# Kernel tuning notes

Hardware: AMD Instinct MI355X
Metric: run time of the kernel (lower is better)

## Reference

```python
import jax, jax.numpy as jnp
import numpy as np

R, C, B, E, H = 128, 256, 1, 768, 12
DK = E // H

def setup_inputs() -> dict:
    key = jax.random.key(0)
    ks = jax.random.split(key, 5)
    s = 1.0 / np.sqrt(E)
    return {
        "x": jax.random.normal(ks[0], (R, C, B, E), jnp.float32),
        "Wq": jax.random.normal(ks[1], (E, E), jnp.float32) * s,
        "bq": jnp.zeros((E,), jnp.float32),
        "Wk": jax.random.normal(ks[2], (E, E), jnp.float32) * s,
        "bk": jnp.zeros((E,), jnp.float32),
        "Wv": jax.random.normal(ks[3], (E, E), jnp.float32) * s,
        "bv": jnp.zeros((E,), jnp.float32),
        "Wo": jax.random.normal(ks[4], (E, E), jnp.float32) * s,
        "bo": jnp.zeros((E,), jnp.float32),
    }

def reference(x, Wq, bq, Wk, bk, Wv, bv, Wo, bo):
    n_rows, n_cols, batch, emb = x.shape
    scaling = (DK ** -0.5) / jnp.sqrt(jnp.float32(n_rows))
    # projections (torch Linear: x @ W.T + b)
    q = (x @ Wq.T + bq).reshape(n_rows, n_cols, batch, H, DK) * scaling
    k = (x @ Wk.T + bk).reshape(n_rows, n_cols, batch, H, DK)
    v = (x @ Wv.T + bv).reshape(n_rows, n_cols, batch, H, DK)
    # pooled attention logits: sum over rows r -> [H, B, C, C]
    attn = jnp.einsum('rinhd,rjnhd->hnij', q, k)
    probs = jax.nn.softmax(attn, axis=-1)  # single softmax shared across rows
    # context: [R, C, B, H, DK]
    c = jnp.einsum('hnij,rjnhd->rinhd', probs, v).reshape(n_rows, n_cols, batch, emb)
    out = c @ Wo.T + bo
    return out, probs
```

## Files before the change

kernel.cpp:

```cpp
#include <hip/hip_runtime.h>
#include <math.h>

#define R_  128
#define C_  256
#define E_  768
#define H_  12
#define DK_ 64
#define T_  (R_*C_)
#define RS_ 8
#define LP  40

typedef __attribute__((ext_vector_type(8))) short          bf16x8;
typedef __attribute__((ext_vector_type(4))) float          f32x4;
typedef __attribute__((ext_vector_type(4))) unsigned short u16x4;
typedef __attribute__((ext_vector_type(8))) unsigned short u16x8;

struct HL { unsigned short h, l; };

__device__ __forceinline__ HL split2(float f) {
    HL o;
    unsigned int u = __float_as_uint(f);
    o.h = (unsigned short)(u >> 16);
    float r = f - __uint_as_float(u & 0xFFFF0000u);
    o.l = (unsigned short)(__float_as_uint(r) >> 16);
    return o;
}

__device__ __forceinline__ void gload16(const void* g, void* l) {
    __builtin_amdgcn_global_load_lds(
        (const __attribute__((address_space(1))) unsigned int*)g,
        (__attribute__((address_space(3))) unsigned int*)l,
        16, 0, 0);
}

__global__ __launch_bounds__(256) void split_kernel(
    const float* __restrict__ src,
    unsigned short* __restrict__ h, unsigned short* __restrict__ l)
{
    const size_t i = ((size_t)blockIdx.x * 256 + threadIdx.x) * 8;
    float4 f0 = *(const float4*)(src + i);
    float4 f1 = *(const float4*)(src + i + 4);
    float v[8] = { f0.x, f0.y, f0.z, f0.w, f1.x, f1.y, f1.z, f1.w };
    u16x8 hh, ll;
    #pragma unroll
    for (int j = 0; j < 8; ++j) { HL e = split2(v[j]); hh[j] = e.h; ll[j] = e.l; }
    *(u16x8*)(h + i) = hh;
    *(u16x8*)(l + i) = ll;
}

template<int OMODE>
__global__ __launch_bounds__(256, 2) void gemm_kernel(
    const unsigned short* __restrict__ Ah, const unsigned short* __restrict__ Al,
    const unsigned short* __restrict__ Bh, const unsigned short* __restrict__ Bl,
    const float* __restrict__ bias, float scale,
    float* __restrict__ Y32, unsigned short* __restrict__ Yh, unsigned short* __restrict__ Yl)
{
    __shared__ __align__(16) unsigned short smem[2][16384];

    const int tid  = threadIdx.x;
    const int m0   = blockIdx.x * 128;
    const int n0   = blockIdx.y * 128;
    const int wave = tid >> 6, lane = tid & 63;
    const int wm   = (wave & 1) * 64, wn = (wave >> 1) * 64;
    const int fr   = lane & 15;
    const int kqs  = (((lane >> 4) ^ ((fr >> 1) & 3)) * 8);

    const int lrow = lane >> 2;
    const int gd   = (lane & 3) ^ ((lane >> 3) & 3);
    const unsigned short* gsrc = (wave == 0) ? Ah : (wave == 1) ? Al
                               : (wave == 2) ? Bh : Bl;
    const int rbase = (wave < 2) ? m0 : n0;
    const unsigned short* sp = gsrc + (size_t)(rbase + lrow) * E_ + 8 * gd;
    const int ltoff = wave * 4096;

    f32x4 acc[4][4] = {};

    {
        unsigned short* lt = &smem[0][ltoff];
        #pragma unroll
        for (int i = 0; i < 8; ++i)
            gload16(sp + (size_t)i * 16 * E_, lt + i * 512);
    }

    int cur = 0;
    for (int k0 = 0; k0 < E_; k0 += 32) {
        __syncthreads();
        if (k0 + 32 < E_) {
            unsigned short* lt = &smem[cur ^ 1][ltoff];
            #pragma unroll
            for (int i = 0; i < 8; ++i)
                gload16(sp + k0 + 32 + (size_t)i * 16 * E_, lt + i * 512);
        }
        const unsigned short* AsH = smem[cur];
        const unsigned short* AsL = smem[cur] + 4096;
        const unsigned short* BsH = smem[cur] + 8192;
        const unsigned short* BsL = smem[cur] + 12288;

        bf16x8 a_h[4], a_l[4], b_h[4], b_l[4];
        #pragma unroll
        for (int t = 0; t < 4; ++t) {
            a_h[t] = *(const bf16x8*)&AsH[(wm + t * 16 + fr) * 32 + kqs];
            a_l[t] = *(const bf16x8*)&AsL[(wm + t * 16 + fr) * 32 + kqs];
            b_h[t] = *(const bf16x8*)&BsH[(wn + t * 16 + fr) * 32 + kqs];
            b_l[t] = *(const bf16x8*)&BsL[(wn + t * 16 + fr) * 32 + kqs];
        }
        #pragma unroll
        for (int i = 0; i < 4; ++i)
            #pragma unroll
            for (int j = 0; j < 4; ++j) {
                acc[i][j] = __builtin_amdgcn_mfma_f32_16x16x32_bf16(a_h[i], b_h[j], acc[i][j], 0, 0, 0);
                acc[i][j] = __builtin_amdgcn_mfma_f32_16x16x32_bf16(a_h[i], b_l[j], acc[i][j], 0, 0, 0);
                acc[i][j] = __builtin_amdgcn_mfma_f32_16x16x32_bf16(a_l[i], b_h[j], acc[i][j], 0, 0, 0);
            }
        cur ^= 1;
    }

    float* rep = (float*)&smem[0][0] + wave * 1024;
    const int mr = lane >> 2;
    const int nc = (lane & 3) * 16;
    #pragma unroll
    for (int ti = 0; ti < 4; ++ti) {
        __syncthreads();
        #pragma unroll
        for (int tj = 0; tj < 4; ++tj)
            #pragma unroll
            for (int r = 0; r < 4; ++r)
                rep[((lane >> 4) * 4 + r) * 64 + tj * 16 + fr] = acc[ti][tj][r];
        __syncthreads();
        float v[16];
        #pragma unroll
        for (int c = 0; c < 4; ++c)
            *(float4*)&v[4 * c] = *(const float4*)&rep[mr * 64 + nc + 4 * c];
        const int gm = m0 + wm + ti * 16 + mr;
        const int gn = n0 + wn + nc;
        if constexpr (OMODE == 1) {
            #pragma unroll
            for (int c = 0; c < 4; ++c) {
                float4 bv = *(const float4*)&bias[gn + 4 * c];
                float4 o;
                o.x = (v[4*c+0] + bv.x) * scale; o.y = (v[4*c+1] + bv.y) * scale;
                o.z = (v[4*c+2] + bv.z) * scale; o.w = (v[4*c+3] + bv.w) * scale;
                *(float4*)&Y32[(size_t)gm * E_ + gn + 4 * c] = o;
            }
        } else {
            unsigned short hh[16], ll[16];
            #pragma unroll
            for (int c = 0; c < 4; ++c) {
                float4 bv = *(const float4*)&bias[gn + 4 * c];
                HL e0 = split2((v[4*c+0] + bv.x) * scale);
                HL e1 = split2((v[4*c+1] + bv.y) * scale);
                HL e2 = split2((v[4*c+2] + bv.z) * scale);
                HL e3 = split2((v[4*c+3] + bv.w) * scale);
                hh[4*c+0] = e0.h; ll[4*c+0] = e0.l;
                hh[4*c+1] = e1.h; ll[4*c+1] = e1.l;
                hh[4*c+2] = e2.h; ll[4*c+2] = e2.l;
                hh[4*c+3] = e3.h; ll[4*c+3] = e3.l;
            }
            u16x8 H0, H1, L0, L1;
            #pragma unroll
            for (int j = 0; j < 8; ++j) { H0[j] = hh[j]; H1[j] = hh[8+j]; L0[j] = ll[j]; L1[j] = ll[8+j]; }
            *(u16x8*)&Yh[(size_t)gm * E_ + gn]     = H0;
            *(u16x8*)&Yh[(size_t)gm * E_ + gn + 8] = H1;
            *(u16x8*)&Yl[(size_t)gm * E_ + gn]     = L0;
            *(u16x8*)&Yl[(size_t)gm * E_ + gn + 8] = L1;
        }
    }
}

__global__ __launch_bounds__(256, 2) void attn_mfma(
    const unsigned short* __restrict__ Qh, const unsigned short* __restrict__ Ql,
    const unsigned short* __restrict__ Kh, const unsigned short* __restrict__ Kl,
    float* __restrict__ part)
{
    __shared__ __align__(16) unsigned short smem[2][16384];

    const int tid  = threadIdx.x;
    const int i0   = blockIdx.x * 128;
    const int j0   = blockIdx.y * 128;
    const int hz   = blockIdx.z;
    const int h    = hz >> 3;
    const int rc   = hz & 7;
    const int wave = tid >> 6, lane = tid & 63;
    const int wm   = (wave & 1) * 64, wn = (wave >> 1) * 64;
    const int fr   = lane & 15;
    const int kqs  = (((lane >> 4) ^ ((fr >> 1) & 3)) * 8);

    const int lrow = lane >> 2;
    const int gd   = (lane & 3) ^ ((lane >> 3) & 3);
    const unsigned short* gsrc = (wave == 0) ? Qh : (wave == 1) ? Ql
                               : (wave == 2) ? Kh : Kl;
    const int rbase = (wave < 2) ? i0 : j0;
    const int ltoff = wave * 4096;
    const unsigned short* sp0 =
        gsrc + ((size_t)(rc * 16 * C_) + rbase + lrow) * E_ + h * DK_ + 8 * gd;

    f32x4 acc[4][4] = {};

    {
        unsigned short* lt = &smem[0][ltoff];
        #pragma unroll
        for (int i = 0; i < 8; ++i)
            gload16(sp0 + (size_t)i * 16 * E_, lt + i * 512);
    }

    int cur = 0;
    for (int s = 0; s < 32; ++s) {
        __syncthreads();
        if (s + 1 < 32) {
            const int sn = s + 1;
            const unsigned short* sp =
                sp0 + (size_t)(sn >> 1) * C_ * E_ + (sn & 1) * 32;
            unsigned short* lt = &smem[cur ^ 1][ltoff];
            #pragma unroll
            for (int i = 0; i < 8; ++i)
                gload16(sp + (size_t)i * 16 * E_, lt + i * 512);
        }
        const unsigned short* AsH = smem[cur];
        const unsigned short* AsL = smem[cur] + 4096;
        const unsigned short* BsH = smem[cur] + 8192;
        const unsigned short* BsL = smem[cur] + 12288;

        bf16x8 a_h[4], a_l[4], b_h[4], b_l[4];
        #pragma unroll
        for (int t = 0; t < 4; ++t) {
            a_h[t] = *(const bf16x8*)&AsH[(wm + t * 16 + fr) * 32 + kqs];
            a_l[t] = *(const bf16x8*)&AsL[(wm + t * 16 + fr) * 32 + kqs];
            b_h[t] = *(const bf16x8*)&BsH[(wn + t * 16 + fr) * 32 + kqs];
            b_l[t] = *(const bf16x8*)&BsL[(wn + t * 16 + fr) * 32 + kqs];
        }
        #pragma unroll
        for (int i = 0; i < 4; ++i)
            #pragma unroll
            for (int j = 0; j < 4; ++j) {
                acc[i][j] = __builtin_amdgcn_mfma_f32_16x16x32_bf16(a_h[i], b_h[j], acc[i][j], 0, 0, 0);
                acc[i][j] = __builtin_amdgcn_mfma_f32_16x16x32_bf16(a_h[i], b_l[j], acc[i][j], 0, 0, 0);
                acc[i][j] = __builtin_amdgcn_mfma_f32_16x16x32_bf16(a_l[i], b_h[j], acc[i][j], 0, 0, 0);
            }
        cur ^= 1;
    }

    float* rep = (float*)&smem[0][0] + wave * 1024;
    const int mr = lane >> 2;
    const int nc = (lane & 3) * 16;
    #pragma unroll
    for (int ti = 0; ti < 4; ++ti) {
        __syncthreads();
        #pragma unroll
        for (int tj = 0; tj < 4; ++tj)
            #pragma unroll
            for (int r = 0; r < 4; ++r)
                rep[((lane >> 4) * 4 + r) * 64 + tj * 16 + fr] = acc[ti][tj][r];
        __syncthreads();
        const int gi = i0 + wm + ti * 16 + mr;
        const int gj = j0 + wn + nc;
        #pragma unroll
        for (int c = 0; c < 4; ++c) {
            float4 o = *(const float4*)&rep[mr * 64 + nc + 4 * c];
            *(float4*)&part[((size_t)(rc * H_ + h) * C_ + gi) * C_ + gj + 4 * c] = o;
        }
    }
}

__global__ __launch_bounds__(256) void softmax_split(
    const float* __restrict__ part, float* __restrict__ probs,
    unsigned short* __restrict__ ph, unsigned short* __restrict__ pl)
{
    const int row = blockIdx.x;
    const int j = threadIdx.x;
    const int wave = j >> 6, lane = j & 63;

    float s = 0.0f;
    #pragma unroll
    for (int rcn = 0; rcn < RS_; ++rcn)
        s += part[((size_t)rcn * H_ * C_ + row) * C_ + j];

    float m = s;
    #pragma unroll
    for (int off = 32; off > 0; off >>= 1)
        m = fmaxf(m, __shfl_down(m, off, 64));
    __shared__ float redm[4];
    if (lane == 0) redm[wave] = m;
    __syncthreads();
    m = fmaxf(fmaxf(redm[0], redm[1]), fmaxf(redm[2], redm[3]));

    float e = expf(s - m);
    float t = e;
    #pragma unroll
    for (int off = 32; off > 0; off >>= 1)
        t += __shfl_down(t, off, 64);
    __shared__ float reds[4];
    if (lane == 0) reds[wave] = t;
    __syncthreads();
    t = reds[0] + reds[1] + reds[2] + reds[3];

    float p = e / t;
    probs[(size_t)row * C_ + j] = p;
    HL sp = split2(p);
    ph[(size_t)row * C_ + j] = sp.h;
    pl[(size_t)row * C_ + j] = sp.l;
}

__global__ __launch_bounds__(256, 2) void ctx_mfma(
    const unsigned short* __restrict__ Ph, const unsigned short* __restrict__ Pl,
    const unsigned short* __restrict__ Vh, const unsigned short* __restrict__ Vl,
    unsigned short* __restrict__ Ch, unsigned short* __restrict__ Cl)
{
    __shared__ __align__(16) unsigned short smem[15360];
    unsigned short* PsH = smem;
    unsigned short* PsL = smem + 5120;
    unsigned short* VsH = smem + 10240;
    unsigned short* VsL = smem + 12800;

    const int tid  = threadIdx.x;
    const int i0   = blockIdx.x * 128;
    const int r    = blockIdx.y;
    const int h    = blockIdx.z;
    const int wave = tid >> 6, lane = tid & 63;
    const int wm   = (wave & 1) * 64, wn = (wave >> 1) * 32;
    const int fr   = lane & 15;
    const int kq   = (lane >> 4) * 8;
    const int srow = tid >> 1;
    const int sk   = (tid & 1) * 16;
    const int vjj  = tid & 31;
    const int vdg  = tid >> 5;

    f32x4 acc[4][2] = {};

    for (int s = 0; s < 8; ++s) {
        const int jb = s * 32;
        const size_t pb = ((size_t)(h * C_) + i0 + srow) * C_ + jb + sk;
        *(u16x8*)&PsH[srow * LP + sk]     = *(const u16x8*)&Ph[pb];
        *(u16x8*)&PsH[srow * LP + sk + 8] = *(const u16x8*)&Ph[pb + 8];
        *(u16x8*)&PsL[srow * LP + sk]     = *(const u16x8*)&Pl[pb];
        *(u16x8*)&PsL[srow * LP + sk + 8] = *(const u16x8*)&Pl[pb + 8];
        const size_t vb = ((size_t)(r * C_) + jb + vjj) * E_ + h * DK_ + vdg * 8;
        u16x8 v_h = *(const u16x8*)&Vh[vb];
        u16x8 v_l = *(const u16x8*)&Vl[vb];
        #pragma unroll
        for (int u = 0; u < 8; ++u) {
            VsH[(vdg * 8 + u) * LP + vjj] = v_h[u];
            VsL[(vdg * 8 + u) * LP + vjj] = v_l[u];
        }
        __syncthreads();

        bf16x8 p_h[4], p_l[4], w_h[2], w_l[2];
        #pragma unroll
        for (int t = 0; t < 4; ++t) {
            p_h[t] = *(const bf16x8*)&PsH[(wm + t * 16 + fr) * LP + kq];
            p_l[t] = *(const bf16x8*)&PsL[(wm + t * 16 + fr) * LP + kq];
        }
        #pragma unroll
        for (int t = 0; t < 2; ++t) {
            w_h[t] = *(const bf16x8*)&VsH[(wn + t * 16 + fr) * LP + kq];
            w_l[t] = *(const bf16x8*)&VsL[(wn + t * 16 + fr) * LP + kq];
        }
        #pragma unroll
        for (int i = 0; i < 4; ++i)
            #pragma unroll
            for (int j = 0; j < 2; ++j) {
                acc[i][j] = __builtin_amdgcn_mfma_f32_16x16x32_bf16(p_h[i], w_h[j], acc[i][j], 0, 0, 0);
                acc[i][j] = __builtin_amdgcn_mfma_f32_16x16x32_bf16(p_h[i], w_l[j], acc[i][j], 0, 0, 0);
                acc[i][j] = __builtin_amdgcn_mfma_f32_16x16x32_bf16(p_l[i], w_h[j], acc[i][j], 0, 0, 0);
            }
        __syncthreads();
    }

    float* rep = (float*)smem + wave * 512;
    const int mr = lane >> 2;
    const int nc = (lane & 3) * 8;
    #pragma unroll
    for (int ti = 0; ti < 4; ++ti) {
        __syncthreads();
        #pragma unroll
        for (int tj = 0; tj < 2; ++tj)
            #pragma unroll
            for (int rr = 0; rr < 4; ++rr)
                rep[((lane >> 4) * 4 + rr) * 32 + tj * 16 + fr] = acc[ti][tj][rr];
        __syncthreads();
        float v[8];
        *(float4*)&v[0] = *(const float4*)&rep[mr * 32 + nc];
        *(float4*)&v[4] = *(const float4*)&rep[mr * 32 + nc + 4];
        const int gm = r * C_ + i0 + wm + ti * 16 + mr;
        const int gn = h * DK_ + wn + nc;
        u16x8 H8, L8;
        #pragma unroll
        for (int jj = 0; jj < 8; ++jj) { HL e = split2(v[jj]); H8[jj] = e.h; L8[jj] = e.l; }
        *(u16x8*)&Ch[(size_t)gm * E_ + gn] = H8;
        *(u16x8*)&Cl[(size_t)gm * E_ + gn] = L8;
    }
}

extern "C" void kernel_launch(void* const* d_in, const int* in_sizes, int n_in,
                              void* d_out, int out_size, void* d_ws, size_t ws_size,
                              hipStream_t stream)
{
    (void)in_sizes; (void)n_in; (void)out_size; (void)ws_size;

    const float* x  = (const float*)d_in[0];
    const float* Wq = (const float*)d_in[1];
    const float* bq = (const float*)d_in[2];
    const float* Wk = (const float*)d_in[3];
    const float* bk = (const float*)d_in[4];
    const float* Wv = (const float*)d_in[5];
    const float* bv = (const float*)d_in[6];
    const float* Wo = (const float*)d_in[7];
    const float* bo = (const float*)d_in[8];

    float* out   = (float*)d_out;
    float* probs = out + (size_t)T_ * E_;
    float* part  = out;

    const size_t QN = (size_t)T_ * E_;
    const size_t WN = (size_t)E_ * E_;
    unsigned short* qh = (unsigned short*)d_ws;
    unsigned short* ql = qh + QN;
    unsigned short* kh = ql + QN;
    unsigned short* kl = kh + QN;
    unsigned short* vh = kl + QN;
    unsigned short* vl = vh + QN;
    unsigned short* ph = kh;
    unsigned short* pl = kh + (size_t)H_ * C_ * C_;
    unsigned short* ch = qh;
    unsigned short* cl = ql;

    unsigned short* xh   = (unsigned short*)out;
    unsigned short* xl   = xh + QN;
    unsigned short* wsph = (unsigned short*)probs;
    unsigned short* wspl = wsph + WN;
    unsigned short* woh  = kl;
    unsigned short* wol  = kl + WN;

    const float scaling = 0.125f / sqrtf(128.0f);

    dim3 blk(256);
    const int xblocks = (int)(QN / 2048);
    const int wblocks = (int)(WN / 2048);

    split_kernel<<<dim3(xblocks), blk, 0, stream>>>(x, xh, xl);

    split_kernel<<<dim3(wblocks), blk, 0, stream>>>(Wq, wsph, wspl);
    gemm_kernel<0><<<dim3(T_ / 128, E_ / 128), blk, 0, stream>>>(
        xh, xl, wsph, wspl, bq, scaling, nullptr, qh, ql);

    split_kernel<<<dim3(wblocks), blk, 0, stream>>>(Wk, wsph, wspl);
    gemm_kernel<0><<<dim3(T_ / 128, E_ / 128), blk, 0, stream>>>(
        xh, xl, wsph, wspl, bk, 1.0f, nullptr, kh, kl);

    split_kernel<<<dim3(wblocks), blk, 0, stream>>>(Wv, wsph, wspl);
    gemm_kernel<0><<<dim3(T_ / 128, E_ / 128), blk, 0, stream>>>(
        xh, xl, wsph, wspl, bv, 1.0f, nullptr, vh, vl);

    attn_mfma<<<dim3(C_ / 128, C_ / 128, H_ * RS_), blk, 0, stream>>>(qh, ql, kh, kl, part);

    split_kernel<<<dim3(wblocks), blk, 0, stream>>>(Wo, woh, wol);

    softmax_split<<<dim3(H_ * C_), blk, 0, stream>>>(part, probs, ph, pl);
    ctx_mfma<<<dim3(C_ / 128, R_, H_), blk, 0, stream>>>(ph, pl, vh, vl, ch, cl);

    gemm_kernel<1><<<dim3(T_ / 128, E_ / 128), blk, 0, stream>>>(
        ch, cl, woh, wol, bo, 1.0f, out, nullptr, nullptr);
}
```

Measured before the change: 873.6 us.

## Prefetch two stages ahead with explicit vmcnt waits in GEMM and logits kernels

Restructures the double-buffered main loops of the projection GEMM and the pooled-logits kernel so that two K-tiles are in flight at once. Each iteration waits on partial vmcnt instead of a full __syncthreads drain, reads fragments into registers, then barriers and refills the same buffer with tile t+2 before the MFMAs run. This aims to hide more global-to-LDS latency behind compute, at the cost of an extra barrier per iteration and reliance on hand-placed waitcnt correctness.

```diff
diff --git a/kernel.cpp b/kernel.cpp
--- a/kernel.cpp
+++ b/kernel.cpp
@@ -33,6 +33,11 @@
         16, 0, 0);
 }
 
+#define WAIT_VM8()   asm volatile("s_waitcnt vmcnt(8)"   ::: "memory")
+#define WAIT_VM0()   asm volatile("s_waitcnt vmcnt(0)"   ::: "memory")
+#define WAIT_LGKM0() asm volatile("s_waitcnt lgkmcnt(0)" ::: "memory")
+#define SBAR()       __builtin_amdgcn_s_barrier()
+
 __global__ __launch_bounds__(256) void split_kernel(
     const float* __restrict__ src,
     unsigned short* __restrict__ h, unsigned short* __restrict__ l)
@@ -76,21 +81,22 @@
     f32x4 acc[4][4] = {};
 
     {
-        unsigned short* lt = &smem[0][ltoff];
+        unsigned short* lt0 = &smem[0][ltoff];
         #pragma unroll
         for (int i = 0; i < 8; ++i)
-            gload16(sp + (size_t)i * 16 * E_, lt + i * 512);
-    }
-
-    int cur = 0;
-    for (int k0 = 0; k0 < E_; k0 += 32) {
-        __syncthreads();
-        if (k0 + 32 < E_) {
-            unsigned short* lt = &smem[cur ^ 1][ltoff];
-            #pragma unroll
-            for (int i = 0; i < 8; ++i)
-                gload16(sp + k0 + 32 + (size_t)i * 16 * E_, lt + i * 512);
-        }
+            gload16(sp + (size_t)i * 16 * E_, lt0 + i * 512);
+        unsigned short* lt1 = &smem[1][ltoff];
+        #pragma unroll
+        for (int i = 0; i < 8; ++i)
+            gload16(sp + 32 + (size_t)i * 16 * E_, lt1 + i * 512);
+    }
+
+    const int NT = E_ / 32;
+    for (int t = 0; t < NT; ++t) {
+        if (t < NT - 1) { WAIT_VM8(); } else { WAIT_VM0(); }
+        SBAR();
+
+        const int cur = t & 1;
         const unsigned short* AsH = smem[cur];
         const unsigned short* AsL = smem[cur] + 4096;
         const unsigned short* BsH = smem[cur] + 8192;
@@ -98,12 +104,23 @@
 
         bf16x8 a_h[4], a_l[4], b_h[4], b_l[4];
         #pragma unroll
-        for (int t = 0; t < 4; ++t) {
-            a_h[t] = *(const bf16x8*)&AsH[(wm + t * 16 + fr) * 32 + kqs];
-            a_l[t] = *(const bf16x8*)&AsL[(wm + t * 16 + fr) * 32 + kqs];
-            b_h[t] = *(const bf16x8*)&BsH[(wn + t * 16 + fr) * 32 + kqs];
-            b_l[t] = *(const bf16x8*)&BsL[(wn + t * 16 + fr) * 32 + kqs];
-        }
+        for (int u = 0; u < 4; ++u) {
+            a_h[u] = *(const bf16x8*)&AsH[(wm + u * 16 + fr) * 32 + kqs];
+            a_l[u] = *(const bf16x8*)&AsL[(wm + u * 16 + fr) * 32 + kqs];
+            b_h[u] = *(const bf16x8*)&BsH[(wn + u * 16 + fr) * 32 + kqs];
+            b_l[u] = *(const bf16x8*)&BsL[(wn + u * 16 + fr) * 32 + kqs];
+        }
+        WAIT_LGKM0();
+        SBAR();
+
+        if (t + 2 < NT) {
+            unsigned short* lt = &smem[cur][ltoff];
+            const unsigned short* spn = sp + (t + 2) * 32;
+            #pragma unroll
+            for (int i = 0; i < 8; ++i)
+                gload16(spn + (size_t)i * 16 * E_, lt + i * 512);
+        }
+
         #pragma unroll
         for (int i = 0; i < 4; ++i)
             #pragma unroll
@@ -112,7 +129,6 @@
                 acc[i][j] = __builtin_amdgcn_mfma_f32_16x16x32_bf16(a_h[i], b_l[j], acc[i][j], 0, 0, 0);
                 acc[i][j] = __builtin_amdgcn_mfma_f32_16x16x32_bf16(a_l[i], b_h[j], acc[i][j], 0, 0, 0);
             }
-        cur ^= 1;
     }
 
     float* rep = (float*)&smem[0][0] + wave * 1024;
@@ -197,24 +213,21 @@
     f32x4 acc[4][4] = {};
 
     {
-        unsigned short* lt = &smem[0][ltoff];
+        unsigned short* lt0 = &smem[0][ltoff];
         #pragma unroll
         for (int i = 0; i < 8; ++i)
-            gload16(sp0 + (size_t)i * 16 * E_, lt + i * 512);
-    }
-
-    int cur = 0;
-    for (int s = 0; s < 32; ++s) {
-        __syncthreads();
-        if (s + 1 < 32) {
-            const int sn = s + 1;
-            const unsigned short* sp =
-                sp0 + (size_t)(sn >> 1) * C_ * E_ + (sn & 1) * 32;
-            unsigned short* lt = &smem[cur ^ 1][ltoff];
-            #pragma unroll
-            for (int i = 0; i < 8; ++i)
-                gload16(sp + (size_t)i * 16 * E_, lt + i * 512);
-        }
+            gload16(sp0 + (size_t)i * 16 * E_, lt0 + i * 512);
+        unsigned short* lt1 = &smem[1][ltoff];
+        #pragma unroll
+        for (int i = 0; i < 8; ++i)
+            gload16(sp0 + 32 + (size_t)i * 16 * E_, lt1 + i * 512);
+    }
+
+    for (int t = 0; t < 32; ++t) {
+        if (t < 31) { WAIT_VM8(); } else { WAIT_VM0(); }
+        SBAR();
+
+        const int cur = t & 1;
         const unsigned short* AsH = smem[cur];
         const unsigned short* AsL = smem[cur] + 4096;
         const unsigned short* BsH = smem[cur] + 8192;
@@ -222,12 +235,25 @@
 
         bf16x8 a_h[4], a_l[4], b_h[4], b_l[4];
         #pragma unroll
-        for (int t = 0; t < 4; ++t) {
-            a_h[t] = *(const bf16x8*)&AsH[(wm + t * 16 + fr) * 32 + kqs];
-            a_l[t] = *(const bf16x8*)&AsL[(wm + t * 16 + fr) * 32 + kqs];
-            b_h[t] = *(const bf16x8*)&BsH[(wn + t * 16 + fr) * 32 + kqs];
-            b_l[t] = *(const bf16x8*)&BsL[(wn + t * 16 + fr) * 32 + kqs];
-        }
+        for (int u = 0; u < 4; ++u) {
+            a_h[u] = *(const bf16x8*)&AsH[(wm + u * 16 + fr) * 32 + kqs];
+            a_l[u] = *(const bf16x8*)&AsL[(wm + u * 16 + fr) * 32 + kqs];
+            b_h[u] = *(const bf16x8*)&BsH[(wn + u * 16 + fr) * 32 + kqs];
+            b_l[u] = *(const bf16x8*)&BsL[(wn + u * 16 + fr) * 32 + kqs];
+        }
+        WAIT_LGKM0();
+        SBAR();
+
+        if (t + 2 < 32) {
+            const int sn = t + 2;
+            const unsigned short* spn =
+                sp0 + (size_t)(sn >> 1) * C_ * E_ + (sn & 1) * 32;
+            unsigned short* lt = &smem[cur][ltoff];
+            #pragma unroll
+            for (int i = 0; i < 8; ++i)
+                gload16(spn + (size_t)i * 16 * E_, lt + i * 512);
+        }
+
         #pragma unroll
         for (int i = 0; i < 4; ++i)
             #pragma unroll
@@ -236,7 +262,6 @@
                 acc[i][j] = __builtin_amdgcn_mfma_f32_16x16x32_bf16(a_h[i], b_l[j], acc[i][j], 0, 0, 0);
                 acc[i][j] = __builtin_amdgcn_mfma_f32_16x16x32_bf16(a_l[i], b_h[j], acc[i][j], 0, 0, 0);
             }
-        cur ^= 1;
     }
 
     float* rep = (float*)&smem[0][0] + wave * 1024;
```

New measurement: 922.4 us. +5.6%, slower.

## Fuse weight hi/lo splitting into GEMM and merge QKV projections into one launch

Applied to the files above, without the earlier changes.

The GEMM now reads fp32 weights directly, splits them into bf16 hi/lo pairs on the fly, and writes them into shared memory. This removes the four separate weight-split kernels. The Q, K and V projections become a single launch with an 18-wide y grid that picks the weight, bias, scale and output per block. The cost is more per-thread conversion work and fp32 weight reads inside the K loop, done through register staging rather than async global-to-LDS loads, which may stall the pipeline.

```diff
diff --git a/kernel.cpp b/kernel.cpp
--- a/kernel.cpp
+++ b/kernel.cpp
@@ -49,48 +49,88 @@
 }
 
 template<int OMODE>
-__global__ __launch_bounds__(256, 2) void gemm_kernel(
+__global__ __launch_bounds__(256, 2) void gemm_fused(
     const unsigned short* __restrict__ Ah, const unsigned short* __restrict__ Al,
-    const unsigned short* __restrict__ Bh, const unsigned short* __restrict__ Bl,
-    const float* __restrict__ bias, float scale,
-    float* __restrict__ Y32, unsigned short* __restrict__ Yh, unsigned short* __restrict__ Yl)
+    const float* __restrict__ W0, const float* __restrict__ W1, const float* __restrict__ W2,
+    const float* __restrict__ b0, const float* __restrict__ b1, const float* __restrict__ b2,
+    float qscale, float* __restrict__ Y32,
+    unsigned short* __restrict__ Y0h, unsigned short* __restrict__ Y0l,
+    unsigned short* __restrict__ Y1h, unsigned short* __restrict__ Y1l,
+    unsigned short* __restrict__ Y2h, unsigned short* __restrict__ Y2l)
 {
     __shared__ __align__(16) unsigned short smem[2][16384];
 
-    const int tid  = threadIdx.x;
-    const int m0   = blockIdx.x * 128;
-    const int n0   = blockIdx.y * 128;
+    const int tid = threadIdx.x;
+    const int m0  = blockIdx.x * 128;
+    const int yb  = blockIdx.y;
+    const int sel = yb / 6;
+    const int n0  = (yb % 6) * 128;
+
+    const float* Wsel = (sel == 0) ? W0 : (sel == 1) ? W1 : W2;
+    const float* bsel = (sel == 0) ? b0 : (sel == 1) ? b1 : b2;
+    const float  scl  = (sel == 0) ? qscale : 1.0f;
+    unsigned short* Yh = (sel == 0) ? Y0h : (sel == 1) ? Y1h : Y2h;
+    unsigned short* Yl = (sel == 0) ? Y0l : (sel == 1) ? Y1l : Y2l;
+
     const int wave = tid >> 6, lane = tid & 63;
-    const int wm   = (wave & 1) * 64, wn = (wave >> 1) * 64;
-    const int fr   = lane & 15;
-    const int kqs  = (((lane >> 4) ^ ((fr >> 1) & 3)) * 8);
-
-    const int lrow = lane >> 2;
-    const int gd   = (lane & 3) ^ ((lane >> 3) & 3);
-    const unsigned short* gsrc = (wave == 0) ? Ah : (wave == 1) ? Al
-                               : (wave == 2) ? Bh : Bl;
-    const int rbase = (wave < 2) ? m0 : n0;
-    const unsigned short* sp = gsrc + (size_t)(rbase + lrow) * E_ + 8 * gd;
-    const int ltoff = wave * 4096;
+    const int wm = (wave & 1) * 64, wn = (wave >> 1) * 64;
+    const int fr = lane & 15;
+    const int kqs = (((lane >> 4) ^ ((fr >> 1) & 3)) * 8);
+
+    const int lrow   = lane >> 2;
+    const int gd     = (lane & 3) ^ ((lane >> 3) & 3);
+    const int aplane = wave >> 1;
+    const int rhalf  = (wave & 1) * 64;
+    const unsigned short* asrc = (aplane ? Al : Ah)
+                                 + (size_t)(m0 + rhalf + lrow) * E_ + 8 * gd;
+    const int ltoff = aplane * 4096 + rhalf * 32;
+
+    const int srow  = tid >> 1;
+    const int g0    = (tid & 1) * 2;
+    const float* wrow = Wsel + (size_t)(n0 + srow) * E_ + g0 * 8;
+    const int slot0 = (g0)     ^ ((srow >> 1) & 3);
+    const int slot1 = (g0 + 1) ^ ((srow >> 1) & 3);
+    const int bbase = srow * 32;
+
+    auto stageB = [&](int buf, int k0) {
+        float4 f0 = *(const float4*)(wrow + k0);
+        float4 f1 = *(const float4*)(wrow + k0 + 4);
+        float4 f2 = *(const float4*)(wrow + k0 + 8);
+        float4 f3 = *(const float4*)(wrow + k0 + 12);
+        float va[8] = { f0.x, f0.y, f0.z, f0.w, f1.x, f1.y, f1.z, f1.w };
+        float vb[8] = { f2.x, f2.y, f2.z, f2.w, f3.x, f3.y, f3.z, f3.w };
+        u16x8 h0, l0, h1, l1;
+        #pragma unroll
+        for (int j = 0; j < 8; ++j) { HL e = split2(va[j]); h0[j] = e.h; l0[j] = e.l; }
+        #pragma unroll
+        for (int j = 0; j < 8; ++j) { HL e = split2(vb[j]); h1[j] = e.h; l1[j] = e.l; }
+        *(u16x8*)&smem[buf][8192  + bbase + slot0 * 8] = h0;
+        *(u16x8*)&smem[buf][12288 + bbase + slot0 * 8] = l0;
+        *(u16x8*)&smem[buf][8192  + bbase + slot1 * 8] = h1;
+        *(u16x8*)&smem[buf][12288 + bbase + slot1 * 8] = l1;
+    };
 
     f32x4 acc[4][4] = {};
 
-    {
-        unsigned short* lt = &smem[0][ltoff];
-        #pragma unroll
-        for (int i = 0; i < 8; ++i)
-            gload16(sp + (size_t)i * 16 * E_, lt + i * 512);
-    }
-
-    int cur = 0;
-    for (int k0 = 0; k0 < E_; k0 += 32) {
-        __syncthreads();
-        if (k0 + 32 < E_) {
-            unsigned short* lt = &smem[cur ^ 1][ltoff];
-            #pragma unroll
-            for (int i = 0; i < 8; ++i)
-                gload16(sp + k0 + 32 + (size_t)i * 16 * E_, lt + i * 512);
-        }
+    #pragma unroll
+    for (int i = 0; i < 4; ++i)
+        gload16(asrc + (size_t)i * 16 * E_, &smem[0][ltoff + i * 512]);
+    stageB(0, 0);
+
+    const int NT = E_ / 32;
+    for (int t = 0; t < NT; ++t) {
+        const int cur = t & 1;
+        __syncthreads();
+
+        if (t + 1 < NT) {
+            const int k1 = (t + 1) * 32;
+            #pragma unroll
+            for (int i = 0; i < 4; ++i)
+                gload16(asrc + k1 + (size_t)i * 16 * E_,
+                        &smem[cur ^ 1][ltoff + i * 512]);
+            stageB(cur ^ 1, k1);
+        }
+
         const unsigned short* AsH = smem[cur];
         const unsigned short* AsL = smem[cur] + 4096;
         const unsigned short* BsH = smem[cur] + 8192;
@@ -98,11 +138,11 @@
 
         bf16x8 a_h[4], a_l[4], b_h[4], b_l[4];
         #pragma unroll
-        for (int t = 0; t < 4; ++t) {
-            a_h[t] = *(const bf16x8*)&AsH[(wm + t * 16 + fr) * 32 + kqs];
-            a_l[t] = *(const bf16x8*)&AsL[(wm + t * 16 + fr) * 32 + kqs];
-            b_h[t] = *(const bf16x8*)&BsH[(wn + t * 16 + fr) * 32 + kqs];
-            b_l[t] = *(const bf16x8*)&BsL[(wn + t * 16 + fr) * 32 + kqs];
+        for (int u = 0; u < 4; ++u) {
+            a_h[u] = *(const bf16x8*)&AsH[(wm + u * 16 + fr) * 32 + kqs];
+            a_l[u] = *(const bf16x8*)&AsL[(wm + u * 16 + fr) * 32 + kqs];
+            b_h[u] = *(const bf16x8*)&BsH[(wn + u * 16 + fr) * 32 + kqs];
+            b_l[u] = *(const bf16x8*)&BsL[(wn + u * 16 + fr) * 32 + kqs];
         }
         #pragma unroll
         for (int i = 0; i < 4; ++i)
@@ -112,7 +152,6 @@
                 acc[i][j] = __builtin_amdgcn_mfma_f32_16x16x32_bf16(a_h[i], b_l[j], acc[i][j], 0, 0, 0);
                 acc[i][j] = __builtin_amdgcn_mfma_f32_16x16x32_bf16(a_l[i], b_h[j], acc[i][j], 0, 0, 0);
             }
-        cur ^= 1;
     }
 
     float* rep = (float*)&smem[0][0] + wave * 1024;
@@ -136,21 +175,21 @@
         if constexpr (OMODE == 1) {
             #pragma unroll
             for (int c = 0; c < 4; ++c) {
-                float4 bv = *(const float4*)&bias[gn + 4 * c];
+                float4 bv = *(const float4*)&bsel[gn + 4 * c];
                 float4 o;
-                o.x = (v[4*c+0] + bv.x) * scale; o.y = (v[4*c+1] + bv.y) * scale;
-                o.z = (v[4*c+2] + bv.z) * scale; o.w = (v[4*c+3] + bv.w) * scale;
+                o.x = (v[4*c+0] + bv.x) * scl; o.y = (v[4*c+1] + bv.y) * scl;
+                o.z = (v[4*c+2] + bv.z) * scl; o.w = (v[4*c+3] + bv.w) * scl;
                 *(float4*)&Y32[(size_t)gm * E_ + gn + 4 * c] = o;
             }
         } else {
             unsigned short hh[16], ll[16];
             #pragma unroll
             for (int c = 0; c < 4; ++c) {
-                float4 bv = *(const float4*)&bias[gn + 4 * c];
-                HL e0 = split2((v[4*c+0] + bv.x) * scale);
-                HL e1 = split2((v[4*c+1] + bv.y) * scale);
-                HL e2 = split2((v[4*c+2] + bv.z) * scale);
-                HL e3 = split2((v[4*c+3] + bv.w) * scale);
+                float4 bv = *(const float4*)&bsel[gn + 4 * c];
+                HL e0 = split2((v[4*c+0] + bv.x) * scl);
+                HL e1 = split2((v[4*c+1] + bv.y) * scl);
+                HL e2 = split2((v[4*c+2] + bv.z) * scl);
+                HL e3 = split2((v[4*c+3] + bv.w) * scl);
                 hh[4*c+0] = e0.h; ll[4*c+0] = e0.l;
                 hh[4*c+1] = e1.h; ll[4*c+1] = e1.l;
                 hh[4*c+2] = e2.h; ll[4*c+2] = e2.l;
@@ -411,7 +450,6 @@
     float* part  = out;
 
     const size_t QN = (size_t)T_ * E_;
-    const size_t WN = (size_t)E_ * E_;
     unsigned short* qh = (unsigned short*)d_ws;
     unsigned short* ql = qh + QN;
     unsigned short* kh = ql + QN;
@@ -423,40 +461,25 @@
     unsigned short* ch = qh;
     unsigned short* cl = ql;
 
-    unsigned short* xh   = (unsigned short*)out;
-    unsigned short* xl   = xh + QN;
-    unsigned short* wsph = (unsigned short*)probs;
-    unsigned short* wspl = wsph + WN;
-    unsigned short* woh  = kl;
-    unsigned short* wol  = kl + WN;
+    unsigned short* xh = (unsigned short*)out;
+    unsigned short* xl = xh + QN;
 
     const float scaling = 0.125f / sqrtf(128.0f);
 
     dim3 blk(256);
     const int xblocks = (int)(QN / 2048);
-    const int wblocks = (int)(WN / 2048);
 
     split_kernel<<<dim3(xblocks), blk, 0, stream>>>(x, xh, xl);
 
-    split_kernel<<<dim3(wblocks), blk, 0, stream>>>(Wq, wsph, wspl);
-    gemm_kernel<0><<<dim3(T_ / 128, E_ / 128), blk, 0, stream>>>(
-        xh, xl, wsph, wspl, bq, scaling, nullptr, qh, ql);
-
-    split_kernel<<<dim3(wblocks), blk, 0, stream>>>(Wk, wsph, wspl);
-    gemm_kernel<0><<<dim3(T_ / 128, E_ / 128), blk, 0, stream>>>(
-        xh, xl, wsph, wspl, bk, 1.0f, nullptr, kh, kl);
-
-    split_kernel<<<dim3(wblocks), blk, 0, stream>>>(Wv, wsph, wspl);
-    gemm_kernel<0><<<dim3(T_ / 128, E_ / 128), blk, 0, stream>>>(
-        xh, xl, wsph, wspl, bv, 1.0f, nullptr, vh, vl);
+    gemm_fused<0><<<dim3(T_ / 128, 18), blk, 0, stream>>>(
+        xh, xl, Wq, Wk, Wv, bq, bk, bv, scaling, nullptr,
+        qh, ql, kh, kl, vh, vl);
 
     attn_mfma<<<dim3(C_ / 128, C_ / 128, H_ * RS_), blk, 0, stream>>>(qh, ql, kh, kl, part);
-
-    split_kernel<<<dim3(wblocks), blk, 0, stream>>>(Wo, woh, wol);
-
     softmax_split<<<dim3(H_ * C_), blk, 0, stream>>>(part, probs, ph, pl);
     ctx_mfma<<<dim3(C_ / 128, R_, H_), blk, 0, stream>>>(ph, pl, vh, vl, ch, cl);
 
-    gemm_kernel<1><<<dim3(T_ / 128, E_ / 128), blk, 0, stream>>>(
-        ch, cl, woh, wol, bo, 1.0f, out, nullptr, nullptr);
-}
+    gemm_fused<1><<<dim3(T_ / 128, 6), blk, 0, stream>>>(
+        ch, cl, Wo, Wo, Wo, bo, bo, bo, 1.0f, out,
+        nullptr, nullptr, nullptr, nullptr, nullptr, nullptr);
+}
```

Result: slower. 987.3 us (+13.0%).

## Swizzle block order for XCD locality and double-buffer ctx_mfma loads

Applied to the files above, without the earlier changes.

Flattens the grids of the GEMM, attention and context kernels to 1D and remaps block IDs with an XCD-aware swizzle (bid&7 stride), so that neighbouring tiles sharing operands run on the same chiplet's L2. It also rewrites ctx_mfma to double-buffer its shared memory. P tiles are loaded with gload16 into a swizzled layout, and the next V tile is prefetched into registers while the current MFMAs run. This halves the number of barriers per step and aims to hide global load latency. In exchange it uses more LDS per block, and the hardcoded grid sizes in the swizzle formulas are fragile.

```diff
diff --git a/kernel.cpp b/kernel.cpp
--- a/kernel.cpp
+++ b/kernel.cpp
@@ -57,9 +57,12 @@
 {
     __shared__ __align__(16) unsigned short smem[2][16384];
 
+    const int bid = blockIdx.x;
+    const int swz = (bid & 7) * 192 + (bid >> 3);
+    const int m0  = (swz / 6) * 128;
+    const int n0  = (swz % 6) * 128;
+
     const int tid  = threadIdx.x;
-    const int m0   = blockIdx.x * 128;
-    const int n0   = blockIdx.y * 128;
     const int wave = tid >> 6, lane = tid & 63;
     const int wm   = (wave & 1) * 64, wn = (wave >> 1) * 64;
     const int fr   = lane & 15;
@@ -174,12 +177,16 @@
 {
     __shared__ __align__(16) unsigned short smem[2][16384];
 
+    const int bid = blockIdx.x;
+    const int swz = (bid & 7) * 48 + (bid >> 3);
+    const int hz  = swz >> 2;
+    const int ij  = swz & 3;
+    const int i0  = (ij & 1) * 128;
+    const int j0  = (ij >> 1) * 128;
+    const int h   = hz >> 3;
+    const int rc  = hz & 7;
+
     const int tid  = threadIdx.x;
-    const int i0   = blockIdx.x * 128;
-    const int j0   = blockIdx.y * 128;
-    const int hz   = blockIdx.z;
-    const int h    = hz >> 3;
-    const int rc   = hz & 7;
     const int wave = tid >> 6, lane = tid & 63;
     const int wm   = (wave & 1) * 64, wn = (wave >> 1) * 64;
     const int fr   = lane & 15;
@@ -305,49 +312,76 @@
     const unsigned short* __restrict__ Vh, const unsigned short* __restrict__ Vl,
     unsigned short* __restrict__ Ch, unsigned short* __restrict__ Cl)
 {
-    __shared__ __align__(16) unsigned short smem[15360];
-    unsigned short* PsH = smem;
-    unsigned short* PsL = smem + 5120;
-    unsigned short* VsH = smem + 10240;
-    unsigned short* VsL = smem + 12800;
+    __shared__ __align__(16) unsigned short smem[2][13312];
+
+    const int bid = blockIdx.x;
+    const int swz = (bid & 7) * 384 + (bid >> 3);
+    const int h   = swz >> 8;
+    const int rem = swz & 255;
+    const int r   = rem >> 1;
+    const int i0  = (rem & 1) * 128;
 
     const int tid  = threadIdx.x;
-    const int i0   = blockIdx.x * 128;
-    const int r    = blockIdx.y;
-    const int h    = blockIdx.z;
     const int wave = tid >> 6, lane = tid & 63;
     const int wm   = (wave & 1) * 64, wn = (wave >> 1) * 32;
     const int fr   = lane & 15;
     const int kq   = (lane >> 4) * 8;
-    const int srow = tid >> 1;
-    const int sk   = (tid & 1) * 16;
-    const int vjj  = tid & 31;
-    const int vdg  = tid >> 5;
+    const int kqs  = (((lane >> 4) ^ ((fr >> 1) & 3)) * 8);
+
+    const int lrow   = lane >> 2;
+    const int gd     = (lane & 3) ^ ((lane >> 3) & 3);
+    const int pplane = wave >> 1;
+    const int prhalf = (wave & 1) * 64;
+    const unsigned short* psrc = (pplane ? Pl : Ph)
+        + ((size_t)(h * C_) + i0 + prhalf + lrow) * C_ + 8 * gd;
+    const int ptoff = pplane * 4096 + prhalf * 32;
+
+    const int vjj = tid & 31;
+    const int vdg = tid >> 5;
+    const unsigned short* vhsrc = Vh + ((size_t)(r * C_) + vjj) * E_ + h * DK_ + vdg * 8;
+    const unsigned short* vlsrc = Vl + ((size_t)(r * C_) + vjj) * E_ + h * DK_ + vdg * 8;
 
     f32x4 acc[4][2] = {};
 
+    {
+        #pragma unroll
+        for (int i = 0; i < 4; ++i)
+            gload16(psrc + (size_t)i * 16 * C_, &smem[0][ptoff + i * 512]);
+        u16x8 v_h = *(const u16x8*)vhsrc;
+        u16x8 v_l = *(const u16x8*)vlsrc;
+        #pragma unroll
+        for (int u = 0; u < 8; ++u) {
+            smem[0][8192  + (vdg * 8 + u) * LP + vjj] = v_h[u];
+            smem[0][10752 + (vdg * 8 + u) * LP + vjj] = v_l[u];
+        }
+    }
+
     for (int s = 0; s < 8; ++s) {
-        const int jb = s * 32;
-        const size_t pb = ((size_t)(h * C_) + i0 + srow) * C_ + jb + sk;
-        *(u16x8*)&PsH[srow * LP + sk]     = *(const u16x8*)&Ph[pb];
-        *(u16x8*)&PsH[srow * LP + sk + 8] = *(const u16x8*)&Ph[pb + 8];
-        *(u16x8*)&PsL[srow * LP + sk]     = *(const u16x8*)&Pl[pb];
-        *(u16x8*)&PsL[srow * LP + sk + 8] = *(const u16x8*)&Pl[pb + 8];
-        const size_t vb = ((size_t)(r * C_) + jb + vjj) * E_ + h * DK_ + vdg * 8;
-        u16x8 v_h = *(const u16x8*)&Vh[vb];
-        u16x8 v_l = *(const u16x8*)&Vl[vb];
-        #pragma unroll
-        for (int u = 0; u < 8; ++u) {
-            VsH[(vdg * 8 + u) * LP + vjj] = v_h[u];
-            VsL[(vdg * 8 + u) * LP + vjj] = v_l[u];
-        }
-        __syncthreads();
+        const int cur = s & 1;
+        __syncthreads();
+
+        u16x8 v_h, v_l;
+        const bool pf = (s + 1 < 8);
+        if (pf) {
+            const int jb = (s + 1) * 32;
+            v_h = *(const u16x8*)(vhsrc + (size_t)jb * E_);
+            v_l = *(const u16x8*)(vlsrc + (size_t)jb * E_);
+            #pragma unroll
+            for (int i = 0; i < 4; ++i)
+                gload16(psrc + jb + (size_t)i * 16 * C_,
+                        &smem[cur ^ 1][ptoff + i * 512]);
+        }
+
+        const unsigned short* PsH = smem[cur];
+        const unsigned short* PsL = smem[cur] + 4096;
+        const unsigned short* VsH = smem[cur] + 8192;
+        const unsigned short* VsL = smem[cur] + 10752;
 
         bf16x8 p_h[4], p_l[4], w_h[2], w_l[2];
         #pragma unroll
         for (int t = 0; t < 4; ++t) {
-            p_h[t] = *(const bf16x8*)&PsH[(wm + t * 16 + fr) * LP + kq];
-            p_l[t] = *(const bf16x8*)&PsL[(wm + t * 16 + fr) * LP + kq];
+            p_h[t] = *(const bf16x8*)&PsH[(wm + t * 16 + fr) * 32 + kqs];
+            p_l[t] = *(const bf16x8*)&PsL[(wm + t * 16 + fr) * 32 + kqs];
         }
         #pragma unroll
         for (int t = 0; t < 2; ++t) {
@@ -362,10 +396,17 @@
                 acc[i][j] = __builtin_amdgcn_mfma_f32_16x16x32_bf16(p_h[i], w_l[j], acc[i][j], 0, 0, 0);
                 acc[i][j] = __builtin_amdgcn_mfma_f32_16x16x32_bf16(p_l[i], w_h[j], acc[i][j], 0, 0, 0);
             }
-        __syncthreads();
-    }
-
-    float* rep = (float*)smem + wave * 512;
+
+        if (pf) {
+            #pragma unroll
+            for (int u = 0; u < 8; ++u) {
+                smem[cur ^ 1][8192  + (vdg * 8 + u) * LP + vjj] = v_h[u];
+                smem[cur ^ 1][10752 + (vdg * 8 + u) * LP + vjj] = v_l[u];
+            }
+        }
+    }
+
+    float* rep = (float*)&smem[0][0] + wave * 512;
     const int mr = lane >> 2;
     const int nc = (lane & 3) * 8;
     #pragma unroll
@@ -439,24 +480,24 @@
     split_kernel<<<dim3(xblocks), blk, 0, stream>>>(x, xh, xl);
 
     split_kernel<<<dim3(wblocks), blk, 0, stream>>>(Wq, wsph, wspl);
-    gemm_kernel<0><<<dim3(T_ / 128, E_ / 128), blk, 0, stream>>>(
+    gemm_kernel<0><<<dim3(1536), blk, 0, stream>>>(
         xh, xl, wsph, wspl, bq, scaling, nullptr, qh, ql);
 
     split_kernel<<<dim3(wblocks), blk, 0, stream>>>(Wk, wsph, wspl);
-    gemm_kernel<0><<<dim3(T_ / 128, E_ / 128), blk, 0, stream>>>(
+    gemm_kernel<0><<<dim3(1536), blk, 0, stream>>>(
         xh, xl, wsph, wspl, bk, 1.0f, nullptr, kh, kl);
 
     split_kernel<<<dim3(wblocks), blk, 0, stream>>>(Wv, wsph, wspl);
-    gemm_kernel<0><<<dim3(T_ / 128, E_ / 128), blk, 0, stream>>>(
+    gemm_kernel<0><<<dim3(1536), blk, 0, stream>>>(
         xh, xl, wsph, wspl, bv, 1.0f, nullptr, vh, vl);
 
-    attn_mfma<<<dim3(C_ / 128, C_ / 128, H_ * RS_), blk, 0, stream>>>(qh, ql, kh, kl, part);
+    attn_mfma<<<dim3(384), blk, 0, stream>>>(qh, ql, kh, kl, part);
 
     split_kernel<<<dim3(wblocks), blk, 0, stream>>>(Wo, woh, wol);
 
     softmax_split<<<dim3(H_ * C_), blk, 0, stream>>>(part, probs, ph, pl);
-    ctx_mfma<<<dim3(C_ / 128, R_, H_), blk, 0, stream>>>(ph, pl, vh, vl, ch, cl);
-
-    gemm_kernel<1><<<dim3(T_ / 128, E_ / 128), blk, 0, stream>>>(
+    ctx_mfma<<<dim3(3072), blk, 0, stream>>>(ph, pl, vh, vl, ch, cl);
+
+    gemm_kernel<1><<<dim3(1536), blk, 0, stream>>>(
         ch, cl, woh, wol, bo, 1.0f, out, nullptr, nullptr);
 }
```

Measured after the change: 851.0 us. -2.6%, faster.
